# Kernel tuning notes

Hardware: AMD Instinct MI355X
Metric: run time of the kernel (lower is better)

Reference implementation:

```python
import jax, jax.numpy as jnp
import numpy as np

IN_DIM = 128
OUT_DIM = 256
NUM_F = 8
BATCH = 1024
NUM = IN_DIM * OUT_DIM


def setup_inputs() -> dict:
    key = jax.random.key(0)
    k_x, k_coef, k_bias = jax.random.split(key, 3)
    x = jax.random.normal(k_x, (BATCH, IN_DIM), dtype=jnp.float32)
    grid = jnp.arange(NUM_F, dtype=jnp.float32) + 1.0                      # [num_f]
    coef = jax.random.uniform(k_coef, (NUM, NUM_F), dtype=jnp.float32)     # torch.rand
    scale_base = jnp.ones((NUM,), dtype=jnp.float32)
    scale_sp = jnp.ones((NUM,), dtype=jnp.float32)
    # nn.Linear(out_dim, 1, bias=False).weight has shape [1, out_dim]
    bound = 1.0 / np.sqrt(OUT_DIM)
    bias_w = jax.random.uniform(k_bias, (1, OUT_DIM), dtype=jnp.float32,
                                minval=-bound, maxval=bound)
    return {"x": x, "grid": grid, "coef": coef, "scale_sp": scale_sp,
            "scale_base": scale_base, "bias_w": bias_w}


def reference(x, grid, coef, scale_sp, scale_base, bias_w):
    batch, in_dim = x.shape
    out_dim = bias_w.shape[1]
    num = in_dim * out_dim
    # Replicate x across out_dim: xe[b, o*in_dim + i] = x[b, i]  -> [batch, num]
    xe = jnp.broadcast_to(x[:, None, :], (batch, out_dim, in_dim)).reshape(batch, num)
    base = jax.nn.silu(xe)                                   # [batch, num]
    # sin(grid * x) basis expansion: [batch, num, num_f]
    f = jnp.sin(xe[:, :, None] * grid[None, None, :])
    fout = jnp.einsum('nf,bnf->bn', coef, f)                 # [batch, num]
    fout = scale_sp * fout + scale_base * base               # [batch, num]
    y = fout.reshape(batch, out_dim, in_dim).sum(axis=2)     # [batch, out_dim]
    return y + bias_w                                        # broadcast [1, out_dim]
```

## Files before the change

kernel.cpp:

```cpp
#include <hip/hip_runtime.h>
#include <hip/hip_bf16.h>

#define IN_DIM  128
#define OUT_DIM 256
#define NUM_F   8
#define BATCH   1024

#define BM 16
#define BN 16
#define XPAD 132

typedef __attribute__((ext_vector_type(8))) short short8;
typedef __attribute__((ext_vector_type(4))) float float4v;

static __device__ __forceinline__ unsigned pk2(float a, float b) {
    float2 t; t.x = a; t.y = b;
    __hip_bfloat162 h = __float22bfloat162_rn(t);
    union { __hip_bfloat162 h; unsigned u; } v; v.h = h;
    return v.u;
}

__global__ __launch_bounds__(256, 4)
void slayer_kernel(const float* __restrict__ x,
                   const float* __restrict__ coef,
                   const float* __restrict__ scale_sp,
                   const float* __restrict__ scale_base,
                   const float* __restrict__ bias_w,
                   float* __restrict__ y)
{
    __shared__ float   x_lds[BM * XPAD];
    __shared__ float4v red[3][64];

    const int t  = threadIdx.x;
    const int o0 = blockIdx.x * BN;
    const int b0 = blockIdx.y * BM;

    {
        const float4v* xg = (const float4v*)(x + (size_t)b0 * IN_DIM);
        #pragma unroll
        for (int r = 0; r < 2; ++r) {
            int idx = r * 256 + t;
            int b = idx >> 5, i4 = idx & 31;
            float4v v = xg[idx];
            *(float4v*)&x_lds[b * XPAD + i4 * 4] = v;
        }
    }
    __syncthreads();

    const int wave = t >> 6, lane = t & 63;
    const int mrow = lane & 15, q = lane >> 4;
    const int m  = mrow;
    const int nn = o0 + mrow;

    const float* xrow = &x_lds[m * XPAD];

    float4v acc = {0.f, 0.f, 0.f, 0.f};

    #pragma unroll 4
    for (int cc = 0; cc < 8; ++cc) {
        const int c = wave + 4 * cc;
        const int i = c * 4 + q;
        const size_t nidx = (size_t)nn * IN_DIM + i;

        const float4v* cg = (const float4v*)(coef + nidx * NUM_F);
        float4v c0 = cg[0], c1 = cg[1];
        float sp = scale_sp[nidx];

        float xv = xrow[i];
        float s1 = __sinf(xv), cs = __cosf(xv);
        float c2 = cs + cs;
        float s2 = c2 * s1;
        float s3 = c2 * s2 - s1;
        float s4 = c2 * s3 - s2;
        float s5 = c2 * s4 - s3;
        float s6 = c2 * s5 - s4;
        float s7 = c2 * s6 - s5;
        float s8 = c2 * s7 - s6;

        union { short8 s; unsigned u[4]; } af, bf;
        af.u[0] = pk2(s1, s2); af.u[1] = pk2(s3, s4);
        af.u[2] = pk2(s5, s6); af.u[3] = pk2(s7, s8);
        bf.u[0] = pk2(c0.x * sp, c0.y * sp); bf.u[1] = pk2(c0.z * sp, c0.w * sp);
        bf.u[2] = pk2(c1.x * sp, c1.y * sp); bf.u[3] = pk2(c1.z * sp, c1.w * sp);

        acc = __builtin_amdgcn_mfma_f32_16x16x32_bf16(af.s, bf.s, acc, 0, 0, 0);
    }

    {
        const int i0 = wave * 32 + q * 8;
        float4v xa = *(const float4v*)&xrow[i0];
        float4v xb = *(const float4v*)&xrow[i0 + 4];
        const float4v* sb = (const float4v*)(scale_base + (size_t)nn * IN_DIM + i0);
        float4v g0 = sb[0], g1 = sb[1];

        float s[8] = {xa.x, xa.y, xa.z, xa.w, xb.x, xb.y, xb.z, xb.w};
        #pragma unroll
        for (int j = 0; j < 8; ++j) s[j] = s[j] / (1.f + __expf(-s[j]));

        union { short8 s; unsigned u[4]; } af, bf;
        af.u[0] = pk2(s[0], s[1]); af.u[1] = pk2(s[2], s[3]);
        af.u[2] = pk2(s[4], s[5]); af.u[3] = pk2(s[6], s[7]);
        bf.u[0] = pk2(g0.x, g0.y); bf.u[1] = pk2(g0.z, g0.w);
        bf.u[2] = pk2(g1.x, g1.y); bf.u[3] = pk2(g1.z, g1.w);

        acc = __builtin_amdgcn_mfma_f32_16x16x32_bf16(af.s, bf.s, acc, 0, 0, 0);
    }

    if (wave > 0) red[wave - 1][lane] = acc;
    __syncthreads();
    if (wave == 0) {
        float4v r0 = red[0][lane], r1 = red[1][lane], r2 = red[2][lane];
        acc.x += r0.x + r1.x + r2.x;
        acc.y += r0.y + r1.y + r2.y;
        acc.z += r0.z + r1.z + r2.z;
        acc.w += r0.w + r1.w + r2.w;

        const float bias = bias_w[nn];
        #pragma unroll
        for (int r = 0; r < 4; ++r) {
            int brow = b0 + q * 4 + r;
            y[(size_t)brow * OUT_DIM + nn] = acc[r] + bias;
        }
    }
}

extern "C" void kernel_launch(void* const* d_in, const int* in_sizes, int n_in,
                              void* d_out, int out_size, void* d_ws, size_t ws_size,
                              hipStream_t stream) {
    const float* x          = (const float*)d_in[0];
    const float* coef       = (const float*)d_in[2];
    const float* scale_sp   = (const float*)d_in[3];
    const float* scale_base = (const float*)d_in[4];
    const float* bias_w     = (const float*)d_in[5];
    float* y = (float*)d_out;

    dim3 grid(OUT_DIM / BN, BATCH / BM);
    slayer_kernel<<<grid, 256, 0, stream>>>(x, coef, scale_sp, scale_base, bias_w, y);
}
```

Before: 75.74 us.

## Split into prep kernel building bf16 feature/weight matrices and a plain GEMM

The fused kernel is replaced by two kernels. The first precomputes the bf16 sin-harmonic and SiLU features of x (once per batch element, rather than once per output tile) and the scaled bf16 weights into a K=1152 workspace. The second is a simple MFMA GEMM over K with a cross-wave reduction. This removes the redundant per-tile transcendental and conversion work, at the cost of a second launch and a global-memory round trip through the workspace. The prep kernel's stores are strided 2-byte writes, which may coalesce poorly.

```diff
diff --git a/kernel.cpp b/kernel.cpp
--- a/kernel.cpp
+++ b/kernel.cpp
@@ -5,10 +5,7 @@
 #define OUT_DIM 256
 #define NUM_F   8
 #define BATCH   1024
-
-#define BM 16
-#define BN 16
-#define XPAD 132
+#define KDIM    1152
 
 typedef __attribute__((ext_vector_type(8))) short short8;
 typedef __attribute__((ext_vector_type(4))) float float4v;
@@ -20,53 +17,35 @@
     return v.u;
 }
 
-__global__ __launch_bounds__(256, 4)
-void slayer_kernel(const float* __restrict__ x,
-                   const float* __restrict__ coef,
-                   const float* __restrict__ scale_sp,
-                   const float* __restrict__ scale_base,
-                   const float* __restrict__ bias_w,
-                   float* __restrict__ y)
+__global__ __launch_bounds__(256)
+void prep_kernel(const float* __restrict__ x,
+                 const float* __restrict__ coef,
+                 const float* __restrict__ scale_sp,
+                 const float* __restrict__ scale_base,
+                 unsigned short* __restrict__ Wb,
+                 unsigned short* __restrict__ Xb)
 {
-    __shared__ float   x_lds[BM * XPAD];
-    __shared__ float4v red[3][64];
+    const int t = threadIdx.x;
+    const int bid = blockIdx.x;
+    union { unsigned u; unsigned short h[2]; } p;
 
-    const int t  = threadIdx.x;
-    const int o0 = blockIdx.x * BN;
-    const int b0 = blockIdx.y * BM;
-
-    {
-        const float4v* xg = (const float4v*)(x + (size_t)b0 * IN_DIM);
-        #pragma unroll
-        for (int r = 0; r < 2; ++r) {
-            int idx = r * 256 + t;
-            int b = idx >> 5, i4 = idx & 31;
-            float4v v = xg[idx];
-            *(float4v*)&x_lds[b * XPAD + i4 * 4] = v;
-        }
-    }
-    __syncthreads();
-
-    const int wave = t >> 6, lane = t & 63;
-    const int mrow = lane & 15, q = lane >> 4;
-    const int m  = mrow;
-    const int nn = o0 + mrow;
-
-    const float* xrow = &x_lds[m * XPAD];
-
-    float4v acc = {0.f, 0.f, 0.f, 0.f};
-
-    #pragma unroll 4
-    for (int cc = 0; cc < 8; ++cc) {
-        const int c = wave + 4 * cc;
-        const int i = c * 4 + q;
-        const size_t nidx = (size_t)nn * IN_DIM + i;
-
-        const float4v* cg = (const float4v*)(coef + nidx * NUM_F);
+    if (bid < 128) {
+        const int n = bid * 256 + t;
+        const int o = n >> 7, i = n & 127;
+        const float4v* cg = (const float4v*)(coef + (size_t)n * NUM_F);
         float4v c0 = cg[0], c1 = cg[1];
-        float sp = scale_sp[nidx];
-
-        float xv = xrow[i];
+        const float sp = scale_sp[n];
+        const float sb = scale_base[n];
+        unsigned short* w = Wb + (size_t)o * KDIM + i;
+        p.u = pk2(c0.x * sp, c0.y * sp); w[0 * IN_DIM] = p.h[0]; w[1 * IN_DIM] = p.h[1];
+        p.u = pk2(c0.z * sp, c0.w * sp); w[2 * IN_DIM] = p.h[0]; w[3 * IN_DIM] = p.h[1];
+        p.u = pk2(c1.x * sp, c1.y * sp); w[4 * IN_DIM] = p.h[0]; w[5 * IN_DIM] = p.h[1];
+        p.u = pk2(c1.z * sp, c1.w * sp); w[6 * IN_DIM] = p.h[0]; w[7 * IN_DIM] = p.h[1];
+        p.u = pk2(sb, 0.f);              w[8 * IN_DIM] = p.h[0];
+    } else {
+        const int idx = (bid - 128) * 256 + t;
+        const int b = idx >> 7, i = idx & 127;
+        const float xv = x[idx];
         float s1 = __sinf(xv), cs = __cosf(xv);
         float c2 = cs + cs;
         float s2 = c2 * s1;
@@ -76,34 +55,39 @@
         float s6 = c2 * s5 - s4;
         float s7 = c2 * s6 - s5;
         float s8 = c2 * s7 - s6;
+        float sil = xv / (1.f + __expf(-xv));
+        unsigned short* xo = Xb + (size_t)b * KDIM + i;
+        p.u = pk2(s1, s2);  xo[0 * IN_DIM] = p.h[0]; xo[1 * IN_DIM] = p.h[1];
+        p.u = pk2(s3, s4);  xo[2 * IN_DIM] = p.h[0]; xo[3 * IN_DIM] = p.h[1];
+        p.u = pk2(s5, s6);  xo[4 * IN_DIM] = p.h[0]; xo[5 * IN_DIM] = p.h[1];
+        p.u = pk2(s7, s8);  xo[6 * IN_DIM] = p.h[0]; xo[7 * IN_DIM] = p.h[1];
+        p.u = pk2(sil, 0.f); xo[8 * IN_DIM] = p.h[0];
+    }
+}
 
-        union { short8 s; unsigned u[4]; } af, bf;
-        af.u[0] = pk2(s1, s2); af.u[1] = pk2(s3, s4);
-        af.u[2] = pk2(s5, s6); af.u[3] = pk2(s7, s8);
-        bf.u[0] = pk2(c0.x * sp, c0.y * sp); bf.u[1] = pk2(c0.z * sp, c0.w * sp);
-        bf.u[2] = pk2(c1.x * sp, c1.y * sp); bf.u[3] = pk2(c1.z * sp, c1.w * sp);
+__global__ __launch_bounds__(256, 4)
+void gemm_kernel(const unsigned short* __restrict__ Xb,
+                 const unsigned short* __restrict__ Wb,
+                 const float* __restrict__ bias_w,
+                 float* __restrict__ y)
+{
+    __shared__ float4v red[3][64];
+    const int t = threadIdx.x;
+    const int o0 = blockIdx.x * 16;
+    const int b0 = blockIdx.y * 16;
+    const int wave = t >> 6, lane = t & 63;
+    const int mrow = lane & 15, q = lane >> 4;
+    const int nn = o0 + mrow;
 
-        acc = __builtin_amdgcn_mfma_f32_16x16x32_bf16(af.s, bf.s, acc, 0, 0, 0);
-    }
+    const unsigned short* aP = Xb + (size_t)(b0 + mrow) * KDIM + wave * 288 + q * 8;
+    const unsigned short* bP = Wb + (size_t)nn * KDIM + wave * 288 + q * 8;
 
-    {
-        const int i0 = wave * 32 + q * 8;
-        float4v xa = *(const float4v*)&xrow[i0];
-        float4v xb = *(const float4v*)&xrow[i0 + 4];
-        const float4v* sb = (const float4v*)(scale_base + (size_t)nn * IN_DIM + i0);
-        float4v g0 = sb[0], g1 = sb[1];
-
-        float s[8] = {xa.x, xa.y, xa.z, xa.w, xb.x, xb.y, xb.z, xb.w};
-        #pragma unroll
-        for (int j = 0; j < 8; ++j) s[j] = s[j] / (1.f + __expf(-s[j]));
-
-        union { short8 s; unsigned u[4]; } af, bf;
-        af.u[0] = pk2(s[0], s[1]); af.u[1] = pk2(s[2], s[3]);
-        af.u[2] = pk2(s[4], s[5]); af.u[3] = pk2(s[6], s[7]);
-        bf.u[0] = pk2(g0.x, g0.y); bf.u[1] = pk2(g0.z, g0.w);
-        bf.u[2] = pk2(g1.x, g1.y); bf.u[3] = pk2(g1.z, g1.w);
-
-        acc = __builtin_amdgcn_mfma_f32_16x16x32_bf16(af.s, bf.s, acc, 0, 0, 0);
+    float4v acc = {0.f, 0.f, 0.f, 0.f};
+    #pragma unroll
+    for (int ks = 0; ks < 9; ++ks) {
+        short8 a = *(const short8*)(aP + ks * 32);
+        short8 b = *(const short8*)(bP + ks * 32);
+        acc = __builtin_amdgcn_mfma_f32_16x16x32_bf16(a, b, acc, 0, 0, 0);
     }
 
     if (wave > 0) red[wave - 1][lane] = acc;
@@ -134,6 +118,11 @@
     const float* bias_w     = (const float*)d_in[5];
     float* y = (float*)d_out;
 
-    dim3 grid(OUT_DIM / BN, BATCH / BM);
-    slayer_kernel<<<grid, 256, 0, stream>>>(x, coef, scale_sp, scale_base, bias_w, y);
+    unsigned short* Wb = (unsigned short*)d_ws;
+    unsigned short* Xb = Wb + (size_t)OUT_DIM * KDIM;
+
+    prep_kernel<<<640, 256, 0, stream>>>(x, coef, scale_sp, scale_base, Wb, Xb);
+
+    dim3 grid(OUT_DIM / 16, BATCH / 16);
+    gemm_kernel<<<grid, 256, 0, stream>>>(Xb, Wb, bias_w, y);
 }
```

New measurement: 75.88 us. Within noise of the previous version (+0.2%).
